# Performance work log

Hardware: AMD Instinct MI355X
Metric: run time of the kernel (lower is better)

The kernel has to match this reference:

```python
import jax, jax.numpy as jnp
import numpy as np

B, N, DIM = 2, 512, 512
HEADS, DIM_HEAD, MAX_LEN = 8, 64, 1024


def _skew(QEr):
    # pad last dim on the left by 1, reshape (n, n+1) -> (n+1, n), drop first row
    padded = jnp.pad(QEr, ((0, 0), (0, 0), (0, 0), (1, 0)))
    b, h, r, c = padded.shape
    return padded.reshape(b, h, c, r)[:, :, 1:, :]


def _fft_multiply_parallel(A, x):
    # A: [b,h,n,n] decay matrix; x: [b,h,n,d]
    b, h, n, d = x.shape
    # y = [last column of A, first row of A] -> [b,h,2n]
    y = jnp.concatenate([A[:, :, :, -1], A[:, :, 0, :]], axis=-1)
    v = jnp.concatenate([x, jnp.zeros_like(x)], axis=-2)  # zero-pad rows n -> 2n
    # Faithful to the original torch code: fftn over ALL axes (incl. batch/head),
    # then ifft over the LAST axis only, then slice back to n rows.
    H = jnp.fft.fftn(y)[:, :, :, None] * jnp.fft.fftn(v)
    return jnp.fft.ifft(H)[:, :, :n, :]


def _forward(x, Wq, Wk, Wv, Er):
    b, n, _ = x.shape

    def split_heads(t):
        return t.reshape(b, n, HEADS, DIM_HEAD).transpose(0, 2, 1, 3)  # [b,h,n,d]

    q = split_heads(x @ Wq)
    k = split_heads(x @ Wk)
    v = split_heads(x @ Wv)
    # global (Frobenius) norm over the full tensor, as torch.norm(t)
    q = q / jnp.linalg.norm(q)
    k = k / jnp.linalg.norm(k)
    q_ = jax.nn.elu(q)
    k_ = jax.nn.elu(k)

    Er_t = Er[MAX_LEN - n:, :].T        # [d, n]
    QEr = q @ Er_t                       # [b,h,n,n]
    c = jnp.exp(_skew(QEr))              # relative-position decay, [b,h,n,n]

    a_1 = jnp.einsum('bhnx,bhny->bhnxy', k_, v).reshape(b, HEADS, n, DIM_HEAD * DIM_HEAD)
    d_2 = _fft_multiply_parallel(c, k_)                                   # [b,h,n,d] complex
    d_1 = _fft_multiply_parallel(c, a_1).reshape(b, HEADS, n, DIM_HEAD, DIM_HEAD)

    top = jnp.einsum('bhnx,bhnyz->bhnz', q_, d_1)    # complex [b,h,n,d]
    bottom = jnp.einsum('bhnx,bhny->bhny', q_, d_2)  # complex [b,h,n,d]
    return top / bottom


def setup_inputs() -> dict:
    key = jax.random.key(0)
    k1, k2, k3, k4, k5 = jax.random.split(key, 5)
    s = jnp.float32(1.0 / np.sqrt(DIM))
    return {
        'x': jax.random.normal(k1, (B, N, DIM), dtype=jnp.float32),
        'Wq': jax.random.normal(k2, (DIM, HEADS * DIM_HEAD), dtype=jnp.float32) * s,
        'Wk': jax.random.normal(k3, (DIM, HEADS * DIM_HEAD), dtype=jnp.float32) * s,
        'Wv': jax.random.normal(k4, (DIM, HEADS * DIM_HEAD), dtype=jnp.float32) * s,
        'Er': jax.random.normal(k5, (MAX_LEN, DIM_HEAD), dtype=jnp.float32),
    }


def reference(x, Wq, Wk, Wv, Er):
    return _forward(x, Wq, Wk, Wv, Er)
```

## Files before the change

kernel.cpp:

```cpp
#include <hip/hip_runtime.h>
#include <math.h>


#define DIMX 512
#define NPOS 512
#define PADIDX(m) ((m) + ((m) >> 4))

typedef unsigned short ushort_t;
typedef unsigned int uint_t;
typedef __bf16 bf16x8 __attribute__((ext_vector_type(8)));
typedef float floatx4 __attribute__((ext_vector_type(4)));

static __device__ inline ushort_t f2bf(float f) {
    uint_t u = __float_as_uint(f);
    u = u + 0x7FFFu + ((u >> 16) & 1u);
    return (ushort_t)(u >> 16);
}
static __device__ inline float bf2f(ushort_t h) {
    return __uint_as_float(((uint_t)h) << 16);
}

#define BFLY(lo, hi, tw) do {                                   \
    const float sr_ = (lo).x - (hi).x, si_ = (lo).y - (hi).y;   \
    (lo).x += (hi).x; (lo).y += (hi).y;                         \
    (hi).x = sr_ * (tw).x - si_ * (tw).y;                       \
    (hi).y = sr_ * (tw).y + si_ * (tw).x;                       \
} while (0)

__global__ __launch_bounds__(256)
void conv_kernel(const float* __restrict__ x,
                 const float* __restrict__ Wk, const float* __restrict__ Wv,
                 ushort_t* __restrict__ xh, ushort_t* __restrict__ xl,
                 ushort_t* __restrict__ wth, ushort_t* __restrict__ wtl,
                 float2* __restrict__ twd)
{
    const int blk = blockIdx.x;
    const int t = threadIdx.x;
    if (blk < 512) {
        const int idx4 = blk * 256 + t;
        const float4 v = ((const float4*)x)[idx4];
        const float vf[4] = {v.x, v.y, v.z, v.w};
        ushort_t h[4], l[4];
        #pragma unroll
        for (int e = 0; e < 4; ++e) {
            h[e] = f2bf(vf[e]);
            l[e] = f2bf(vf[e] - bf2f(h[e]));
        }
        ushort_t* ph = xh + (size_t)idx4 * 4;
        ushort_t* pl = xl + (size_t)idx4 * 4;
        #pragma unroll
        for (int e = 0; e < 4; ++e) { ph[e] = h[e]; pl[e] = l[e]; }
    } else if (blk < 1024) {
        __shared__ float tile[32][33];
        const int b2 = blk - 512;
        const int s  = b2 >> 8;
        const int kt = (b2 >> 4) & 15;
        const int nt = b2 & 15;
        const int c  = t & 31, r4 = t >> 5;
        const float* __restrict__ W = s ? Wv : Wk;
        #pragma unroll
        for (int i = 0; i < 4; ++i) {
            const int row = r4 + i * 8;
            tile[row][c] = W[(size_t)(kt * 32 + row) * 512 + nt * 32 + c];
        }
        __syncthreads();
        #pragma unroll
        for (int i = 0; i < 4; ++i) {
            const int nl = r4 + i * 8;
            const float v = tile[c][nl];
            const ushort_t h = f2bf(v);
            const ushort_t l = f2bf(v - bf2f(h));
            const size_t o = (size_t)(s * 512 + nt * 32 + nl) * 512 + kt * 32 + c;
            wth[o] = h;
            wtl[o] = l;
        }
    } else {
        const int jj = (blk - 1024) * 256 + t;
        double s, cc;
        sincos(-6.2831853071795864769 * (double)jj / 1024.0, &s, &cc);
        twd[jj] = make_float2((float)cc, (float)s);
    }
}

__global__ __launch_bounds__(256)
void gemm_mfma_kernel(const ushort_t* __restrict__ xh, const ushort_t* __restrict__ xl,
                      const ushort_t* __restrict__ wth, const ushort_t* __restrict__ wtl,
                      float* __restrict__ K, float* __restrict__ V,
                      float* __restrict__ partials)
{
    const int blk = blockIdx.x;
    const int ct = blk >> 5;
    const int rt = blk & 31;
    const int t = threadIdx.x;
    const int w = t >> 6, lane = t & 63;
    const int qd = lane >> 4, lm = lane & 15;
    const int mrow  = rt * 32 + (w >> 1) * 16 + lm;
    const int ncol0 = ct * 64 + (w & 1) * 32;
    const size_t aoff  = (size_t)mrow * 512 + qd * 8;
    const size_t boff0 = (size_t)(ncol0 + lm) * 512 + qd * 8;
    const size_t boff1 = (size_t)(ncol0 + 16 + lm) * 512 + qd * 8;

    floatx4 acc0 = {0.f, 0.f, 0.f, 0.f};
    floatx4 acc1 = {0.f, 0.f, 0.f, 0.f};

    #pragma unroll
    for (int ks = 0; ks < 16; ++ks) {
        const int k0 = ks * 32;
        const bf16x8 Ah  = *(const bf16x8*)&xh [aoff  + k0];
        const bf16x8 Al  = *(const bf16x8*)&xl [aoff  + k0];
        const bf16x8 B0h = *(const bf16x8*)&wth[boff0 + k0];
        const bf16x8 B0l = *(const bf16x8*)&wtl[boff0 + k0];
        const bf16x8 B1h = *(const bf16x8*)&wth[boff1 + k0];
        const bf16x8 B1l = *(const bf16x8*)&wtl[boff1 + k0];
        acc0 = __builtin_amdgcn_mfma_f32_16x16x32_bf16(Ah, B0h, acc0, 0, 0, 0);
        acc0 = __builtin_amdgcn_mfma_f32_16x16x32_bf16(Ah, B0l, acc0, 0, 0, 0);
        acc0 = __builtin_amdgcn_mfma_f32_16x16x32_bf16(Al, B0h, acc0, 0, 0, 0);
        acc1 = __builtin_amdgcn_mfma_f32_16x16x32_bf16(Ah, B1h, acc1, 0, 0, 0);
        acc1 = __builtin_amdgcn_mfma_f32_16x16x32_bf16(Ah, B1l, acc1, 0, 0, 0);
        acc1 = __builtin_amdgcn_mfma_f32_16x16x32_bf16(Al, B1h, acc1, 0, 0, 0);
    }

    __shared__ float red[4];
    float ss = 0.f;
    const int orow0 = rt * 32 + (w >> 1) * 16 + qd * 4;
    float* __restrict__ O = (ct < 8) ? K : V;
    const int cb = (ct < 8) ? 0 : 512;
    const int c0 = ncol0 + lm - cb;
    #pragma unroll
    for (int r = 0; r < 4; ++r) {
        const size_t row = orow0 + r;
        const float v0 = acc0[r], v1 = acc1[r];
        O[row * 512 + c0]      = v0;
        O[row * 512 + c0 + 16] = v1;
        if (ct < 8) ss += v0 * v0 + v1 * v1;
    }
    #pragma unroll
    for (int off = 32; off > 0; off >>= 1)
        ss += __shfl_down(ss, off, 64);
    if (lane == 0) red[w] = ss;
    __syncthreads();
    if (t == 0) partials[blk] = red[0] + red[1] + red[2] + red[3];
}

__device__ __constant__ float C8[8] = {
    1.f, 0.70710678118654752440f, 0.f, -0.70710678118654752440f,
   -1.f, -0.70710678118654752440f, 0.f, 0.70710678118654752440f };
__device__ __constant__ float S8[8] = {
    0.f, -0.70710678118654752440f, -1.f, -0.70710678118654752440f,
    0.f,  0.70710678118654752440f,  1.f,  0.70710678118654752440f };

__global__ __launch_bounds__(256)
void stage1_kernel(const float* __restrict__ K,
                   const float* __restrict__ V,
                   const float* __restrict__ partials,
                   float2* __restrict__ Gk,
                   float2* __restrict__ Gp)
{
    const int m = blockIdx.x;
    const int t = threadIdx.x;
    __shared__ float kk[2][8][64];
    __shared__ float pp[2][8][64];
    __shared__ float skp[16][4];
    __shared__ float sk[2][8];
    __shared__ float sred[4];

    float p = partials[t] + partials[t + 256];
    #pragma unroll
    for (int off = 32; off > 0; off >>= 1)
        p += __shfl_down(p, off, 64);
    if ((t & 63) == 0) sred[t >> 6] = p;
    __syncthreads();
    const float scale = (float)(1.0 / sqrt((double)sred[0] + (double)sred[1] +
                                           (double)sred[2] + (double)sred[3]));

    {
        const int e0 = t * 4;
        const int b = e0 >> 9, rem = e0 & 511, h = rem >> 6, z = rem & 63;
        const size_t src = (size_t)(b * 512 + m) * DIMX + h * 64 + z;
        const float4 kv4 = *(const float4*)&K[src];
        const float4 vv4 = *(const float4*)&V[src];
        const float kf[4] = {kv4.x, kv4.y, kv4.z, kv4.w};
        const float vf[4] = {vv4.x, vv4.y, vv4.z, vv4.w};
        #pragma unroll
        for (int e = 0; e < 4; ++e) {
            const float kv = kf[e] * scale;
            kk[b][h][z + e] = kv > 0.f ? kv : expm1f(kv);
            pp[b][h][z + e] = vf[e];
        }
    }
    __syncthreads();
    if (t < 64) {
        const int bh = t >> 2, q = t & 3;
        float s = 0.f;
        #pragma unroll
        for (int zz = 0; zz < 16; ++zz) s += kk[bh >> 3][bh & 7][q * 16 + zz];
        skp[bh][q] = s;
    }
    __syncthreads();
    if (t < 16) sk[t >> 3][t & 7] = skp[t][0] + skp[t][1] + skp[t][2] + skp[t][3];
    __syncthreads();
    for (int e = t; e < 1024; e += 256) {
        const int b = e >> 9, rem = e & 511, h = rem >> 6, z = rem & 63;
        pp[b][h][z] *= sk[b][h];
    }
    __syncthreads();

    for (int e2 = t; e2 < 512; e2 += 256) {
        const int be = e2 >> 5;
        const int zp = e2 & 31;
        const int beta = be >> 3, eta = be & 7;
        float4 rk, rp;
        #pragma unroll
        for (int zz = 0; zz < 2; ++zz) {
            const int z = zp * 2 + zz;
            float gkr = 0.f, gki = 0.f, gpr = 0.f, gpi = 0.f;
            #pragma unroll
            for (int b = 0; b < 2; ++b) {
                const float sgn = (beta & b) ? -1.f : 1.f;
                #pragma unroll
                for (int h = 0; h < 8; ++h) {
                    const int ph = (eta * h) & 7;
                    const float cr = C8[ph], ci = S8[ph];
                    const float a = kk[b][h][z] * sgn;
                    gkr = fmaf(a, cr, gkr); gki = fmaf(a, ci, gki);
                    const float p2 = pp[b][h][z] * sgn;
                    gpr = fmaf(p2, cr, gpr); gpi = fmaf(p2, ci, gpi);
                }
            }
            if (zz == 0) { rk.x = gkr; rk.y = gki; rp.x = gpr; rp.y = gpi; }
            else         { rk.z = gkr; rk.w = gki; rp.z = gpr; rp.w = gpi; }
        }
        const size_t o = ((size_t)be * NPOS + m) * 64 + zp * 2;
        *(float4*)&Gk[o] = rk;
        *(float4*)&Gp[o] = rp;
    }
}

__global__ __launch_bounds__(256)
void fft_div_kernel(const float2* __restrict__ Gk,
                    const float2* __restrict__ Gp,
                    const float2* __restrict__ twd,
                    float* __restrict__ out, int out_cplx)
{
    const int blk = blockIdx.x;
    const int j  = blk & 7;
    const int l  = (blk >> 3) & 3;
    const int be = blk >> 5;
    const int zg = j * 4 + l;
    const int t  = threadIdx.x;

    __shared__ float2 g[4][1088];
    __shared__ float2 w[544];

    for (int jj = t; jj < 512; jj += 256)
        w[PADIDX(jj)] = twd[jj];
    __syncthreads();

    for (int e = t; e < 1024; e += 256) {
        const int a = e >> 9;
        const int m = e & 511;
        const float4 v4 = *(const float4*)&(a ? Gp : Gk)[((size_t)be * NPOS + m) * 64 + zg * 2];
        const float2 v0 = make_float2(v4.x, v4.y);
        const float2 v1 = make_float2(v4.z, v4.w);
        const float2 tw = w[PADIDX(m)];
        g[a * 2 + 0][PADIDX(m)] = v0;
        g[a * 2 + 1][PADIDX(m)] = v1;
        g[a * 2 + 0][PADIDX(m + 512)] = make_float2(v0.x * tw.x - v0.y * tw.y,
                                                    v0.x * tw.y + v0.y * tw.x);
        g[a * 2 + 1][PADIDX(m + 512)] = make_float2(v1.x * tw.x - v1.y * tw.y,
                                                    v1.x * tw.y + v1.y * tw.x);
    }
    __syncthreads();

    const int wv   = t >> 6;
    const int lane = t & 63;

    #pragma unroll
    for (int q = 0; q < 2; ++q) {
        const int arr = wv;
        const int h   = q;
        const int jo  = lane;
        float2 f[8];
        #pragma unroll
        for (int k = 0; k < 8; ++k)
            f[k] = g[arr][PADIDX(h * 512 + jo + k * 64)];
        #pragma unroll
        for (int k = 0; k < 4; ++k) {
            const float2 tw = w[PADIDX(2 * jo + 128 * k)];
            BFLY(f[k], f[k + 4], tw);
        }
        {
            const float2 tw0 = w[PADIDX(4 * jo)];
            const float2 tw1 = w[PADIDX(4 * jo + 256)];
            BFLY(f[0], f[2], tw0); BFLY(f[1], f[3], tw1);
            BFLY(f[4], f[6], tw0); BFLY(f[5], f[7], tw1);
        }
        {
            const float2 tw = w[PADIDX(8 * jo)];
            BFLY(f[0], f[1], tw); BFLY(f[2], f[3], tw);
            BFLY(f[4], f[5], tw); BFLY(f[6], f[7], tw);
        }
        #pragma unroll
        for (int k = 0; k < 8; ++k)
            g[arr][PADIDX(h * 512 + jo + k * 64)] = f[k];
    }
    __syncthreads();

    #pragma unroll
    for (int q = 0; q < 2; ++q) {
        const int arr = wv;
        const int b64 = q * 8 + (lane >> 3);
        const int jo  = lane & 7;
        const int e0  = b64 * 64 + jo;
        float2 f[8];
        #pragma unroll
        for (int k = 0; k < 8; ++k)
            f[k] = g[arr][PADIDX(e0 + 8 * k)];
        #pragma unroll
        for (int k = 0; k < 4; ++k) {
            const float2 tw = w[PADIDX(16 * jo + 128 * k)];
            BFLY(f[k], f[k + 4], tw);
        }
        {
            const float2 tw0 = w[PADIDX(32 * jo)];
            const float2 tw1 = w[PADIDX(32 * jo + 256)];
            BFLY(f[0], f[2], tw0); BFLY(f[1], f[3], tw1);
            BFLY(f[4], f[6], tw0); BFLY(f[5], f[7], tw1);
        }
        {
            const float2 tw = w[PADIDX(64 * jo)];
            BFLY(f[0], f[1], tw); BFLY(f[2], f[3], tw);
            BFLY(f[4], f[5], tw); BFLY(f[6], f[7], tw);
        }
        #pragma unroll
        for (int k = 0; k < 8; ++k)
            g[arr][PADIDX(e0 + 8 * k)] = f[k];
    }
    __syncthreads();

    #pragma unroll
    for (int q = 0; q < 2; ++q) {
        const int arr = wv;
        const int b8  = q * 64 + lane;
        const int e0  = b8 * 8;
        float2 f[8];
        #pragma unroll
        for (int k = 0; k < 8; ++k)
            f[k] = g[arr][PADIDX(e0 + k)];
        BFLY(f[0], f[4], w[PADIDX(0)]);
        BFLY(f[1], f[5], w[PADIDX(128)]);
        BFLY(f[2], f[6], w[PADIDX(256)]);
        BFLY(f[3], f[7], w[PADIDX(384)]);
        {
            const float2 tw0 = w[PADIDX(0)];
            const float2 tw1 = w[PADIDX(256)];
            BFLY(f[0], f[2], tw0); BFLY(f[1], f[3], tw1);
            BFLY(f[4], f[6], tw0); BFLY(f[5], f[7], tw1);
        }
        f[0].x += f[1].x; f[0].y += f[1].y;
        f[2].x += f[3].x; f[2].y += f[3].y;
        f[4].x += f[5].x; f[4].y += f[5].y;
        f[6].x += f[7].x; f[6].y += f[7].y;
        g[arr][PADIDX(e0 + 0)] = f[0];
        g[arr][PADIDX(e0 + 2)] = f[2];
        g[arr][PADIDX(e0 + 4)] = f[4];
        g[arr][PADIDX(e0 + 6)] = f[6];
    }
    __syncthreads();

    for (int e2 = t; e2 < 512; e2 += 256) {
        const int i  = e2;
        const int pi = PADIDX(2 * i);
        const int mu = (int)(__brev((unsigned)i) >> 23);
        float4 res;
        #pragma unroll
        for (int zi = 0; zi < 2; ++zi) {
            const float2 D  = g[zi][pi];
            const float2 Nm = g[2 + zi][pi];
            const float inv = 1.f / (D.x * D.x + D.y * D.y);
            const float rr = (Nm.x * D.x + Nm.y * D.y) * inv;
            const float ri = (Nm.y * D.x - Nm.x * D.y) * inv;
            if (zi == 0) { res.x = rr; res.y = ri; }
            else         { res.z = rr; res.w = ri; }
        }
        const size_t o = ((size_t)be * NPOS + mu) * 64 + zg * 2;
        if (out_cplx) {
            *(float4*)&((float2*)out)[o] = res;
        } else {
            out[o]     = res.x;
            out[o + 1] = res.z;
        }
    }
}

__global__ __launch_bounds__(256)
void gemm_kv_kernel(const float* __restrict__ x,
                    const float* __restrict__ Wk,
                    const float* __restrict__ Wv,
                    float* __restrict__ K,
                    float* __restrict__ V,
                    float* __restrict__ partials)
{
    const int blk  = blockIdx.x;
    const int sel  = (blk >> 2) & 1;
    const int cg2  = blk & 3;
    const int rt   = blk >> 3;
    const int row0 = rt * 16;
    const int col0 = cg2 * 128;
    const int t    = threadIdx.x;
    const int tc   = t & 31;
    const int tr   = t >> 5;
    const float* __restrict__ W   = sel ? Wv : Wk;
    float* __restrict__       Out = sel ? V  : K;

    __shared__ float xs[16][DIMX];
    __shared__ float red[4];

    #pragma unroll
    for (int j = 0; j < 8; ++j) {
        const int f = t + j * 256;
        const int row = f >> 7, c4 = f & 127;
        *(float4*)&xs[row][c4 * 4] = *(const float4*)&x[(size_t)(row0 + row) * DIMX + c4 * 4];
    }
    __syncthreads();

    const float* Wb = W + col0 + tc * 4;
    float4 wA[8], wB[8];
    #pragma unroll
    for (int j = 0; j < 8; ++j) wA[j] = *(const float4*)&Wb[(size_t)(j) * DIMX];
    #pragma unroll
    for (int j = 0; j < 8; ++j) wB[j] = *(const float4*)&Wb[(size_t)(8 + j) * DIMX];

    float acc[2][4] = {{0,0,0,0},{0,0,0,0}};
    const int r0 = tr * 2;

    #define COMPUTE_CHUNK(WREG, CH)                                            \
        {   float4 xv0a = *(const float4*)&xs[r0][(CH) * 8];                   \
            float4 xv0b = *(const float4*)&xs[r0][(CH) * 8 + 4];               \
            float4 xv1a = *(const float4*)&xs[r0 + 1][(CH) * 8];               \
            float4 xv1b = *(const float4*)&xs[r0 + 1][(CH) * 8 + 4];           \
            _Pragma("unroll")                                                  \
            for (int kk = 0; kk < 4; ++kk) {                                   \
                const float x0 = (&xv0a.x)[kk], x1 = (&xv1a.x)[kk];            \
                _Pragma("unroll")                                              \
                for (int cc = 0; cc < 4; ++cc) {                               \
                    acc[0][cc] = fmaf(x0, (&WREG[kk].x)[cc], acc[0][cc]);      \
                    acc[1][cc] = fmaf(x1, (&WREG[kk].x)[cc], acc[1][cc]);      \
                } }                                                            \
            _Pragma("unroll")                                                  \
            for (int kk = 0; kk < 4; ++kk) {                                   \
                const float x0 = (&xv0b.x)[kk], x1 = (&xv1b.x)[kk];            \
                _Pragma("unroll")                                              \
                for (int cc = 0; cc < 4; ++cc) {                               \
                    acc[0][cc] = fmaf(x0, (&WREG[kk + 4].x)[cc], acc[0][cc]);  \
                    acc[1][cc] = fmaf(x1, (&WREG[kk + 4].x)[cc], acc[1][cc]);  \
                } } }

    for (int ch = 0; ch < 64; ch += 2) {
        COMPUTE_CHUNK(wA, ch)
        if (ch < 62) {
            #pragma unroll
            for (int j = 0; j < 8; ++j)
                wA[j] = *(const float4*)&Wb[(size_t)((ch + 2) * 8 + j) * DIMX];
        }
        COMPUTE_CHUNK(wB, ch + 1)
        if (ch < 62) {
            #pragma unroll
            for (int j = 0; j < 8; ++j)
                wB[j] = *(const float4*)&Wb[(size_t)((ch + 3) * 8 + j) * DIMX];
        }
    }
    #undef COMPUTE_CHUNK

    float ss = 0.f;
    #pragma unroll
    for (int i = 0; i < 2; ++i) {
        const int row = row0 + r0 + i;
        const float4 o = make_float4(acc[i][0], acc[i][1], acc[i][2], acc[i][3]);
        *(float4*)&Out[(size_t)row * DIMX + col0 + tc * 4] = o;
        ss += o.x * o.x + o.y * o.y + o.z * o.z + o.w * o.w;
    }
    if (sel == 0) {
        #pragma unroll
        for (int off = 32; off > 0; off >>= 1)
            ss += __shfl_down(ss, off, 64);
        if ((t & 63) == 0) red[t >> 6] = ss;
        __syncthreads();
        if (t == 0) partials[blk] = red[0] + red[1] + red[2] + red[3];
    } else {
        if (t == 0) partials[blk] = 0.f;
    }
}

__global__ __launch_bounds__(256)
void mdft_fallback_kernel(const float2* __restrict__ Gk,
                          const float2* __restrict__ Gp,
                          float* __restrict__ out,
                          int out_cplx)
{
    const int blk = blockIdx.x;
    const int be = blk >> 6, z = blk & 63;
    const int t = threadIdx.x;
    __shared__ float2 gk[512];
    __shared__ float2 gp[512];
    __shared__ float2 w[1024];

    for (int m = t; m < 512; m += 256) {
        const size_t idx = ((size_t)be * NPOS + m) * 64 + z;
        gk[m] = Gk[idx];
        gp[m] = Gp[idx];
    }
    for (int jj = t; jj < 1024; jj += 256) {
        double s, c;
        sincos(-6.2831853071795864769 * (double)jj / 1024.0, &s, &c);
        w[jj] = make_float2((float)c, (float)s);
    }
    __syncthreads();

    #pragma unroll
    for (int half = 0; half < 2; ++half) {
        const int mu = t + half * 256;
        double dr = 0.0, di = 0.0, nr = 0.0, ni = 0.0;
        int idx = 0;
        for (int m = 0; m < 512; ++m) {
            const float2 tw = w[idx];
            idx = (idx + mu) & 1023;
            const float2 a = gk[m];
            dr += (double)(a.x * tw.x - a.y * tw.y);
            di += (double)(a.x * tw.y + a.y * tw.x);
            const float2 p = gp[m];
            nr += (double)(p.x * tw.x - p.y * tw.y);
            ni += (double)(p.x * tw.y + p.y * tw.x);
        }
        const double dmag = dr * dr + di * di;
        const double orr = (nr * dr + ni * di) / dmag;
        const double oii = (ni * dr - nr * di) / dmag;
        const size_t o = ((size_t)be * NPOS + mu) * 64 + z;
        if (out_cplx) {
            out[2 * o]     = (float)orr;
            out[2 * o + 1] = (float)oii;
        } else {
            out[o] = (float)orr;
        }
    }
}

extern "C" void kernel_launch(void* const* d_in, const int* in_sizes, int n_in,
                              void* d_out, int out_size, void* d_ws, size_t ws_size,
                              hipStream_t stream)
{
    const float* x  = (const float*)d_in[0];
    const float* Wk = (const float*)d_in[2];
    const float* Wv = (const float*)d_in[3];
    float* out = (float*)d_out;

    char* ws = (char*)d_ws;
    float*  K    = (float*)(ws);
    float*  V    = (float*)(ws + (size_t)2097152);
    float2* Gk   = (float2*)(ws + (size_t)4194304);
    float*  part = (float*)(ws + (size_t)8388608);
    const int out_cplx = (out_size >= 2 * 2 * 8 * 512 * 64) ? 1 : 0;

    const bool ws_big = (ws_size >= (size_t)20971520);
    float2* Gp = ws_big ? (float2*)(ws + (size_t)8390656)
                        : (float2*)d_out;

    if (ws_big) {
        ushort_t* xh  = (ushort_t*)(ws + (size_t)16777216);
        ushort_t* xl  = (ushort_t*)(ws + (size_t)17825792);
        ushort_t* wth = (ushort_t*)(ws + (size_t)18874368);
        ushort_t* wtl = (ushort_t*)(ws + (size_t)19922944);
        float2*   twd = (float2*)(ws + (size_t)12584960);
        hipLaunchKernelGGL(conv_kernel, dim3(1026), dim3(256), 0, stream,
                           x, Wk, Wv, xh, xl, wth, wtl, twd);
        hipLaunchKernelGGL(gemm_mfma_kernel, dim3(512), dim3(256), 0, stream,
                           xh, xl, wth, wtl, K, V, part);
        hipLaunchKernelGGL(stage1_kernel, dim3(512), dim3(256), 0, stream,
                           K, V, part, Gk, Gp);
        hipLaunchKernelGGL(fft_div_kernel, dim3(512), dim3(256), 0, stream,
                           Gk, Gp, twd, out, out_cplx);
    } else {
        hipLaunchKernelGGL(gemm_kv_kernel, dim3(512), dim3(256), 0, stream,
                           x, Wk, Wv, K, V, part);
        hipLaunchKernelGGL(stage1_kernel, dim3(512), dim3(256), 0, stream,
                           K, V, part, Gk, Gp);
        hipLaunchKernelGGL(mdft_fallback_kernel, dim3(1024), dim3(256), 0, stream,
                           Gk, Gp, out, out_cplx);
    }
}
```

Baseline: 105.8 us.

## Vectorize bf16 stores, fold sk scaling into DFT, drop FFT barriers

```diff
diff --git a/kernel.cpp b/kernel.cpp
--- a/kernel.cpp
+++ b/kernel.cpp
@@ -46,10 +46,10 @@
             h[e] = f2bf(vf[e]);
             l[e] = f2bf(vf[e] - bf2f(h[e]));
         }
-        ushort_t* ph = xh + (size_t)idx4 * 4;
-        ushort_t* pl = xl + (size_t)idx4 * 4;
-        #pragma unroll
-        for (int e = 0; e < 4; ++e) { ph[e] = h[e]; pl[e] = l[e]; }
+        const ushort4 hv4 = make_ushort4(h[0], h[1], h[2], h[3]);
+        const ushort4 lv4 = make_ushort4(l[0], l[1], l[2], l[3]);
+        *(ushort4*)(xh + (size_t)idx4 * 4) = hv4;
+        *(ushort4*)(xl + (size_t)idx4 * 4) = lv4;
     } else if (blk < 1024) {
         __shared__ float tile[32][33];
         const int b2 = blk - 512;
@@ -199,37 +199,35 @@
     __syncthreads();
     if (t < 16) sk[t >> 3][t & 7] = skp[t][0] + skp[t][1] + skp[t][2] + skp[t][3];
     __syncthreads();
-    for (int e = t; e < 1024; e += 256) {
-        const int b = e >> 9, rem = e & 511, h = rem >> 6, z = rem & 63;
-        pp[b][h][z] *= sk[b][h];
-    }
-    __syncthreads();
 
     for (int e2 = t; e2 < 512; e2 += 256) {
         const int be = e2 >> 5;
         const int zp = e2 & 31;
         const int beta = be >> 3, eta = be & 7;
-        float4 rk, rp;
-        #pragma unroll
-        for (int zz = 0; zz < 2; ++zz) {
-            const int z = zp * 2 + zz;
-            float gkr = 0.f, gki = 0.f, gpr = 0.f, gpi = 0.f;
+        float kr[2] = {0.f, 0.f}, ki[2] = {0.f, 0.f};
+        float pr[2] = {0.f, 0.f}, pim[2] = {0.f, 0.f};
+        #pragma unroll
+        for (int b = 0; b < 2; ++b) {
+            const float sgn = (beta & b) ? -1.f : 1.f;
             #pragma unroll
-            for (int b = 0; b < 2; ++b) {
-                const float sgn = (beta & b) ? -1.f : 1.f;
+            for (int h = 0; h < 8; ++h) {
+                const int ph = (eta * h) & 7;
+                const float cr = C8[ph], ci = S8[ph];
+                const float skv = sk[b][h];
                 #pragma unroll
-                for (int h = 0; h < 8; ++h) {
-                    const int ph = (eta * h) & 7;
-                    const float cr = C8[ph], ci = S8[ph];
+                for (int zz = 0; zz < 2; ++zz) {
+                    const int z = zp * 2 + zz;
                     const float a = kk[b][h][z] * sgn;
-                    gkr = fmaf(a, cr, gkr); gki = fmaf(a, ci, gki);
-                    const float p2 = pp[b][h][z] * sgn;
-                    gpr = fmaf(p2, cr, gpr); gpi = fmaf(p2, ci, gpi);
+                    kr[zz] = fmaf(a, cr, kr[zz]);
+                    ki[zz] = fmaf(a, ci, ki[zz]);
+                    const float p2 = (pp[b][h][z] * skv) * sgn;
+                    pr[zz]  = fmaf(p2, cr, pr[zz]);
+                    pim[zz] = fmaf(p2, ci, pim[zz]);
                 }
             }
-            if (zz == 0) { rk.x = gkr; rk.y = gki; rp.x = gpr; rp.y = gpi; }
-            else         { rk.z = gkr; rk.w = gki; rp.z = gpr; rp.w = gpi; }
-        }
+        }
+        const float4 rk = make_float4(kr[0], ki[0], kr[1], ki[1]);
+        const float4 rp = make_float4(pr[0], pim[0], pr[1], pim[1]);
         const size_t o = ((size_t)be * NPOS + m) * 64 + zp * 2;
         *(float4*)&Gk[o] = rk;
         *(float4*)&Gp[o] = rp;
@@ -304,7 +302,6 @@
         for (int k = 0; k < 8; ++k)
             g[arr][PADIDX(h * 512 + jo + k * 64)] = f[k];
     }
-    __syncthreads();
 
     #pragma unroll
     for (int q = 0; q < 2; ++q) {
@@ -336,7 +333,6 @@
         for (int k = 0; k < 8; ++k)
             g[arr][PADIDX(e0 + 8 * k)] = f[k];
     }
-    __syncthreads();
 
     #pragma unroll
     for (int q = 0; q < 2; ++q) {
@@ -417,8 +413,8 @@
     __shared__ float red[4];
 
     #pragma unroll
-    for (int j = 0; j < 8; ++j) {
-        const int f = t + j * 256;
+    for (int jj = 0; jj < 8; ++jj) {
+        const int f = t + jj * 256;
         const int row = f >> 7, c4 = f & 127;
         *(float4*)&xs[row][c4 * 4] = *(const float4*)&x[(size_t)(row0 + row) * DIMX + c4 * 4];
     }
@@ -427,9 +423,9 @@
     const float* Wb = W + col0 + tc * 4;
     float4 wA[8], wB[8];
     #pragma unroll
-    for (int j = 0; j < 8; ++j) wA[j] = *(const float4*)&Wb[(size_t)(j) * DIMX];
-    #pragma unroll
-    for (int j = 0; j < 8; ++j) wB[j] = *(const float4*)&Wb[(size_t)(8 + j) * DIMX];
+    for (int jj = 0; jj < 8; ++jj) wA[jj] = *(const float4*)&Wb[(size_t)(jj) * DIMX];
+    #pragma unroll
+    for (int jj = 0; jj < 8; ++jj) wB[jj] = *(const float4*)&Wb[(size_t)(8 + jj) * DIMX];
 
     float acc[2][4] = {{0,0,0,0},{0,0,0,0}};
     const int r0 = tr * 2;
@@ -460,14 +456,14 @@
         COMPUTE_CHUNK(wA, ch)
         if (ch < 62) {
             #pragma unroll
-            for (int j = 0; j < 8; ++j)
-                wA[j] = *(const float4*)&Wb[(size_t)((ch + 2) * 8 + j) * DIMX];
+            for (int jj = 0; jj < 8; ++jj)
+                wA[jj] = *(const float4*)&Wb[(size_t)((ch + 2) * 8 + jj) * DIMX];
         }
         COMPUTE_CHUNK(wB, ch + 1)
         if (ch < 62) {
             #pragma unroll
-            for (int j = 0; j < 8; ++j)
-                wB[j] = *(const float4*)&Wb[(size_t)((ch + 3) * 8 + j) * DIMX];
+            for (int jj = 0; jj < 8; ++jj)
+                wB[jj] = *(const float4*)&Wb[(size_t)((ch + 3) * 8 + jj) * DIMX];
         }
     }
     #undef COMPUTE_CHUNK
@@ -528,9 +524,9 @@
             const float2 a = gk[m];
             dr += (double)(a.x * tw.x - a.y * tw.y);
             di += (double)(a.x * tw.y + a.y * tw.x);
-            const float2 p = gp[m];
-            nr += (double)(p.x * tw.x - p.y * tw.y);
-            ni += (double)(p.x * tw.y + p.y * tw.x);
+            const float2 p2 = gp[m];
+            nr += (double)(p2.x * tw.x - p2.y * tw.y);
+            ni += (double)(p2.x * tw.y + p2.y * tw.x);
         }
         const double dmag = dr * dr + di * di;
         const double orr = (nr * dr + ni * di) / dmag;
```

New measurement: 105.4 us. About the same (-0.4%).
